# Optimization experiments

Measured on AMD Instinct MI355X. Metric: run time of the kernel, lower is better.

## Reference

```python
import jax, jax.numpy as jnp
import numpy as np

N_NODES = 100000
N_EDGES = 1200000
IN_DIM, HID, OUT = 128, 64, 64


def setup_inputs() -> dict:
    key = jax.random.key(0)
    ks = jax.random.split(key, 16)
    s = 0.05
    return {
        "x": jax.random.normal(ks[0], (N_NODES, IN_DIM), jnp.float32),
        "fc_w": jax.random.normal(ks[1], (IN_DIM, HID), jnp.float32) * s,
        "fc_b": jnp.zeros((HID,), jnp.float32),
        "conv1_w": jax.random.normal(ks[2], (IN_DIM, HID), jnp.float32) * s,
        "conv1_b": jnp.zeros((HID,), jnp.float32),
        "fc1_w": jax.random.normal(ks[3], (2 * HID, OUT), jnp.float32) * s,
        "fc1_b": jnp.zeros((OUT,), jnp.float32),
        "conv2_w": jax.random.normal(ks[4], (2 * HID, OUT), jnp.float32) * s,
        "conv2_b": jnp.zeros((OUT,), jnp.float32),
        "fc2_w": jax.random.normal(ks[5], (OUT, 1), jnp.float32) * s,
        "fc2_b": jnp.zeros((1,), jnp.float32),
        "conv3_w": jax.random.normal(ks[6], (OUT, 1), jnp.float32) * s,
        "conv3_b": jnp.zeros((1,), jnp.float32),
        "edge_index": jax.random.randint(ks[7], (2, N_EDGES), 0, N_NODES, jnp.int64 if jax.config.jax_enable_x64 else jnp.int32),
    }


def gcn_conv(h_in, w, b, row, col, norm, n_nodes):
    # PyG GCNConv (no self loops): scatter_add(norm * (XW)[row]) at col, + bias
    h = h_in @ w                                  # [N, F_out]
    msg = h[row] * norm[:, None]                  # [E, F_out]
    out = jax.ops.segment_sum(msg, col, num_segments=n_nodes)
    return out + b


def reference(x, fc_w, fc_b, conv1_w, conv1_b, fc1_w, fc1_b, conv2_w, conv2_b,
              fc2_w, fc2_b, conv3_w, conv3_b, edge_index):
    n = x.shape[0]
    row, col = edge_index[0], edge_index[1]
    # symmetric normalization: deg over destination nodes (unit edge weights)
    deg = jax.ops.segment_sum(jnp.ones(row.shape[0], x.dtype), col, num_segments=n)
    dinv = jnp.where(deg > 0, jax.lax.rsqrt(jnp.maximum(deg, 1.0)), 0.0)
    norm = dinv[row] * dinv[col]                  # [E]

    x1 = jax.nn.relu(x @ fc_w + fc_b)             # MLP branch [N, HID]
    x2 = jax.nn.relu(gcn_conv(x, conv1_w, conv1_b, row, col, norm, n))
    x3 = jnp.concatenate([x1, x2], axis=1)        # [N, 2*HID]
    x5 = jax.nn.relu(x3 @ fc1_w + fc1_b)
    x6 = jax.nn.relu(gcn_conv(x3, conv2_w, conv2_b, row, col, norm, n))
    x7 = x5 + x6                                  # residual combine [N, OUT]
    x9 = x7 @ fc2_w + fc2_b
    x10 = gcn_conv(x7, conv3_w, conv3_b, row, col, norm, n)
    return x9 + x10                               # [N, 1]
```

## Files before the change

### kernel.cpp

```cpp
#include <hip/hip_runtime.h>

#define IN_DIM 128
#define HID 64
#define RB_SHIFT 10
#define RB 1024
#define NBMAX 128
#define MAXBIN 16384
#define PCH 2048

typedef short bf16x8 __attribute__((ext_vector_type(8)));
typedef float f32x4  __attribute__((ext_vector_type(4)));

__device__ __forceinline__ float relu(float v) { return v > 0.f ? v : 0.f; }

__device__ __forceinline__ unsigned short f2bf(float f) {
    unsigned u = __float_as_uint(f);
    u += 0x7FFFu + ((u >> 16) & 1u);
    return (unsigned short)(u >> 16);
}

__device__ __forceinline__ float bflo(unsigned u) { return __uint_as_float(u << 16); }
__device__ __forceinline__ float bfhi(unsigned u) { return __uint_as_float(u & 0xFFFF0000u); }

__global__ void k_initbins(int* __restrict__ binCursor, int NR) {
    if (threadIdx.x < NR) binCursor[threadIdx.x] = threadIdx.x * MAXBIN;
}

__global__ __launch_bounds__(256) void k_wprep(const float* __restrict__ W1a,
                                               const float* __restrict__ W2a,
                                               const float* __restrict__ W1b,
                                               const float* __restrict__ W2b,
                                               unsigned short* __restrict__ Wt) {
    const int t = blockIdx.x * 256 + threadIdx.x;
    if (t >= 2 * 4 * 8 * 64) return;
    const int lane = t & 63;
    const int c = (t >> 6) & 7;
    const int kc = (t >> 9) & 3;
    const int layer = t >> 11;
    const int col = c * 16 + (lane & 15);
    const int k0 = kc * 32 + (lane >> 4) * 8;
    const float* W1 = layer ? W1b : W1a;
    const float* W2 = layer ? W2b : W2a;
    const float* src = (col < 64) ? (W1 + col) : (W2 + (col - 64));
    unsigned short v[8];
#pragma unroll
    for (int j = 0; j < 8; j++) v[j] = f2bf(src[(size_t)(k0 + j) * 64]);
    *(ushort4*)(Wt + (size_t)t * 8) = make_ushort4(v[0], v[1], v[2], v[3]);
    *(ushort4*)(Wt + (size_t)t * 8 + 4) = make_ushort4(v[4], v[5], v[6], v[7]);
}

__global__ __launch_bounds__(256) void k_part(const int* __restrict__ row,
                                              const int* __restrict__ col,
                                              int* __restrict__ binCursor,
                                              int2* __restrict__ part, int E) {
    __shared__ int lcur[NBMAX], gbase[NBMAX];
    const int tid = threadIdx.x;
    const int e0 = blockIdx.x * PCH;
    const int cnt = min(PCH, E - e0);
    if (tid < NBMAX) lcur[tid] = 0;
    __syncthreads();
    int rr[8], cc[8], pp[8];
    if (cnt == PCH) {
#pragma unroll
        for (int h = 0; h < 2; h++) {
            const int4 c4 = *(const int4*)(col + e0 + h * 1024 + tid * 4);
            const int4 r4 = *(const int4*)(row + e0 + h * 1024 + tid * 4);
            cc[h * 4 + 0] = c4.x; cc[h * 4 + 1] = c4.y;
            cc[h * 4 + 2] = c4.z; cc[h * 4 + 3] = c4.w;
            rr[h * 4 + 0] = r4.x; rr[h * 4 + 1] = r4.y;
            rr[h * 4 + 2] = r4.z; rr[h * 4 + 3] = r4.w;
        }
    } else {
#pragma unroll
        for (int j = 0; j < 8; j++) {
            const int e = e0 + j * 256 + tid;
            if (e < e0 + cnt) { rr[j] = row[e]; cc[j] = col[e]; }
            else cc[j] = -1;
        }
    }
#pragma unroll
    for (int j = 0; j < 8; j++)
        if (cc[j] >= 0) pp[j] = atomicAdd(&lcur[cc[j] >> RB_SHIFT], 1);
    __syncthreads();
    if (tid < NBMAX && lcur[tid] > 0)
        gbase[tid] = atomicAdd(&binCursor[tid], lcur[tid]);
    __syncthreads();
#pragma unroll
    for (int j = 0; j < 8; j++)
        if (cc[j] >= 0)
            part[gbase[cc[j] >> RB_SHIFT] + pp[j]] = make_int2(rr[j], cc[j]);
}

__global__ __launch_bounds__(256) void k_hist(const int* __restrict__ binCursor,
                                              const int2* __restrict__ part,
                                              int* __restrict__ degi,
                                              float* __restrict__ dinv, int N) {
    __shared__ int cnt[RB];
    const int b = blockIdx.x;
    const int lo = b << RB_SHIFT;
    const int tid = threadIdx.x;
    for (int i = tid; i < RB; i += 256) cnt[i] = 0;
    __syncthreads();
    const int base = b * MAXBIN;
    const int tot = binCursor[b] - base;
    for (int i = tid; i < tot; i += 256)
        atomicAdd(&cnt[part[base + i].y - lo], 1);
    __syncthreads();
    for (int i = tid; i < RB; i += 256) {
        const int n = lo + i;
        if (n < N) {
            const int d = cnt[i];
            degi[n] = d;
            dinv[n] = d > 0 ? rsqrtf((float)d) : 0.f;
        }
    }
}

__global__ __launch_bounds__(256) void k_scan1(const int* __restrict__ degi,
                                               int* __restrict__ start,
                                               int* __restrict__ bsum, int N) {
    __shared__ int s[256];
    const int tid = threadIdx.x;
    const int i = blockIdx.x * 256 + tid;
    const int v = (i < N) ? degi[i] : 0;
    s[tid] = v;
    __syncthreads();
    for (int off = 1; off < 256; off <<= 1) {
        int t = (tid >= off) ? s[tid - off] : 0;
        __syncthreads();
        s[tid] += t;
        __syncthreads();
    }
    if (i < N) start[i] = s[tid] - v;
    if (tid == 255) bsum[blockIdx.x] = s[255];
}

__global__ __launch_bounds__(512) void k_scan2(int* __restrict__ bsum, int NB) {
    __shared__ int s[512];
    const int tid = threadIdx.x;
    const int v = (tid < NB) ? bsum[tid] : 0;
    s[tid] = v;
    __syncthreads();
    for (int off = 1; off < 512; off <<= 1) {
        int t = (tid >= off) ? s[tid - off] : 0;
        __syncthreads();
        s[tid] += t;
        __syncthreads();
    }
    if (tid < NB) bsum[tid] = s[tid] - v;
}

__global__ __launch_bounds__(256) void k_scan3(int* __restrict__ start,
                                               const int* __restrict__ bsum, int N) {
    int i = blockIdx.x * 256 + threadIdx.x;
    if (i < N) start[i] += bsum[blockIdx.x];
}

__global__ __launch_bounds__(256) void k_bucket3(const int* __restrict__ binCursor,
                                                 const int2* __restrict__ part,
                                                 const int* __restrict__ start,
                                                 const float* __restrict__ dinv,
                                                 int2* __restrict__ rw, int N) {
    __shared__ int curs[RB];
    __shared__ float dv[RB];
    const int b = blockIdx.x;
    const int lo = b << RB_SHIFT;
    const int tid = threadIdx.x;
    for (int i = tid; i < RB; i += 256) {
        const int n = lo + i;
        curs[i] = (n < N) ? start[n] : 0;
        dv[i] = (n < N) ? dinv[n] : 0.f;
    }
    __syncthreads();
    const int base = b * MAXBIN;
    const int tot = binCursor[b] - base;
    for (int i = tid; i < tot; i += 256) {
        const int2 v = part[base + i];
        const int li = v.y - lo;
        const int pos = atomicAdd(&curs[li], 1);
        rw[pos] = make_int2(v.x, __float_as_int(dinv[v.x] * dv[li]));
    }
}

template <int LAYER>
__global__ __launch_bounds__(256) void k_gemm(const float* __restrict__ XA,
                                              const float* __restrict__ XB,
                                              const float* __restrict__ CB,
                                              const unsigned short* __restrict__ Wt,
                                              const float* __restrict__ B1,
                                              float* __restrict__ O1,
                                              unsigned short* __restrict__ O2,
                                              int N) {
    const int tid = threadIdx.x;
    const int wave = tid >> 6;
    const int lane = tid & 63;
    const int quad = lane >> 4;
    const int lm = lane & 15;
    const int n0 = blockIdx.x * 64 + wave * 16;
    if (n0 >= N) return;
    const int nrow = min(n0 + lm, N - 1);

    f32x4 acc[8];
#pragma unroll
    for (int c = 0; c < 8; c++) acc[c] = (f32x4){0.f, 0.f, 0.f, 0.f};

#pragma unroll
    for (int kc = 0; kc < 4; kc++) {
        const int k0 = kc * 32 + quad * 8;
        float4 q0, q1;
        if (LAYER == 1) {
            const float* s = XA + (size_t)nrow * IN_DIM + k0;
            q0 = *(const float4*)s;
            q1 = *(const float4*)(s + 4);
        } else {
            if (kc < 2) {
                const float* s = XA + (size_t)nrow * 64 + k0;
                q0 = *(const float4*)s;
                q1 = *(const float4*)(s + 4);
            } else {
                const int kb = k0 - 64;
                const float* s = XB + (size_t)nrow * 64 + kb;
                q0 = *(const float4*)s;
                q1 = *(const float4*)(s + 4);
                const float4 c0 = *(const float4*)(CB + kb);
                const float4 c1 = *(const float4*)(CB + kb + 4);
                q0.x = relu(q0.x + c0.x); q0.y = relu(q0.y + c0.y);
                q0.z = relu(q0.z + c0.z); q0.w = relu(q0.w + c0.w);
                q1.x = relu(q1.x + c1.x); q1.y = relu(q1.y + c1.y);
                q1.z = relu(q1.z + c1.z); q1.w = relu(q1.w + c1.w);
            }
        }
        bf16x8 a;
        a[0] = (short)f2bf(q0.x); a[1] = (short)f2bf(q0.y);
        a[2] = (short)f2bf(q0.z); a[3] = (short)f2bf(q0.w);
        a[4] = (short)f2bf(q1.x); a[5] = (short)f2bf(q1.y);
        a[6] = (short)f2bf(q1.z); a[7] = (short)f2bf(q1.w);
#pragma unroll
        for (int c = 0; c < 8; c++) {
            const bf16x8 b = *(const bf16x8*)(Wt + (size_t)((kc * 8 + c) * 64 + lane) * 8);
            acc[c] = __builtin_amdgcn_mfma_f32_16x16x32_bf16(a, b, acc[c], 0, 0, 0);
        }
    }

    const int nb = n0 + quad * 4;
#pragma unroll
    for (int c = 0; c < 4; c++) {
        const int col = c * 16 + lm;
        const float b = B1[col];
#pragma unroll
        for (int r = 0; r < 4; r++) {
            const int n = nb + r;
            if (n < N) O1[(size_t)n * 64 + col] = relu(acc[c][r] + b);
        }
    }
#pragma unroll
    for (int c = 4; c < 8; c++) {
        const int col = (c - 4) * 16 + lm;
#pragma unroll
        for (int r = 0; r < 4; r++) {
            const int n = nb + r;
            if (n < N) O2[(size_t)n * 64 + col] = f2bf(acc[c][r]);
        }
    }
}

__global__ __launch_bounds__(256) void k_gather64(const int* __restrict__ start,
                                                  const int* __restrict__ degi,
                                                  const int2* __restrict__ rw,
                                                  const unsigned short* __restrict__ H,
                                                  float* __restrict__ AGG, int N) {
    const int l = threadIdx.x & 15;
    const int d = blockIdx.x * 16 + (threadIdx.x >> 4);
    if (d >= N) return;
    int s = start[d];
    const int e2 = s + degi[d];
    float a0 = 0.f, a1 = 0.f, a2 = 0.f, a3 = 0.f;
    for (; s + 3 < e2; s += 4) {
        const int2 ea = rw[s], eb = rw[s + 1], ec = rw[s + 2], ed = rw[s + 3];
        const uint2 ua = *(const uint2*)(H + (size_t)ea.x * 64 + l * 4);
        const uint2 ub = *(const uint2*)(H + (size_t)eb.x * 64 + l * 4);
        const uint2 uc = *(const uint2*)(H + (size_t)ec.x * 64 + l * 4);
        const uint2 ud = *(const uint2*)(H + (size_t)ed.x * 64 + l * 4);
        const float wa = __int_as_float(ea.y), wb = __int_as_float(eb.y);
        const float wc = __int_as_float(ec.y), wd = __int_as_float(ed.y);
        a0 += wa * bflo(ua.x); a1 += wa * bfhi(ua.x);
        a2 += wa * bflo(ua.y); a3 += wa * bfhi(ua.y);
        a0 += wb * bflo(ub.x); a1 += wb * bfhi(ub.x);
        a2 += wb * bflo(ub.y); a3 += wb * bfhi(ub.y);
        a0 += wc * bflo(uc.x); a1 += wc * bfhi(uc.x);
        a2 += wc * bflo(uc.y); a3 += wc * bfhi(uc.y);
        a0 += wd * bflo(ud.x); a1 += wd * bfhi(ud.x);
        a2 += wd * bflo(ud.y); a3 += wd * bfhi(ud.y);
    }
    for (; s < e2; ++s) {
        const int2 ea = rw[s];
        const uint2 ua = *(const uint2*)(H + (size_t)ea.x * 64 + l * 4);
        const float wa = __int_as_float(ea.y);
        a0 += wa * bflo(ua.x); a1 += wa * bfhi(ua.x);
        a2 += wa * bflo(ua.y); a3 += wa * bfhi(ua.y);
    }
    *(float4*)(AGG + (size_t)d * 64 + l * 4) = make_float4(a0, a1, a2, a3);
}

__global__ __launch_bounds__(256) void k_combine(const float* __restrict__ X5,
                                                 const float* __restrict__ AGG2,
                                                 const float* __restrict__ CB2,
                                                 const float* __restrict__ FC2W,
                                                 const float* __restrict__ FC2B,
                                                 const float* __restrict__ C3W,
                                                 const float* __restrict__ C3B,
                                                 float* __restrict__ H3,
                                                 float* __restrict__ OUT, int N) {
    const int lane = threadIdx.x & 63;
    const int n = blockIdx.x * 4 + (threadIdx.x >> 6);
    if (n >= N) return;
    const size_t o = (size_t)n * 64 + lane;
    const float v = X5[o] + relu(AGG2[o] + CB2[lane]);
    float p9 = v * FC2W[lane];
    float p10 = v * C3W[lane];
#pragma unroll
    for (int s = 32; s >= 1; s >>= 1) {
        p9 += __shfl_xor(p9, s, 64);
        p10 += __shfl_xor(p10, s, 64);
    }
    if (lane == 0) {
        OUT[n] = p9 + FC2B[0] + C3B[0];
        H3[n] = p10;
    }
}

__global__ __launch_bounds__(256) void k_gather1f(const int* __restrict__ start,
                                                  const int* __restrict__ degi,
                                                  const int2* __restrict__ rw,
                                                  const float* __restrict__ H3,
                                                  float* __restrict__ OUT, int N) {
    const int d = blockIdx.x * 256 + threadIdx.x;
    if (d >= N) return;
    int s = start[d];
    const int e2 = s + degi[d];
    float acc = 0.f;
    for (; s + 1 < e2; s += 2) {
        const int2 a = rw[s], b = rw[s + 1];
        acc += H3[a.x] * __int_as_float(a.y);
        acc += H3[b.x] * __int_as_float(b.y);
    }
    if (s < e2) {
        const int2 a = rw[s];
        acc += H3[a.x] * __int_as_float(a.y);
    }
    OUT[d] += acc;
}

extern "C" void kernel_launch(void* const* d_in, const int* in_sizes, int n_in,
                              void* d_out, int out_size, void* d_ws, size_t ws_size,
                              hipStream_t stream) {
    const float* x    = (const float*)d_in[0];
    const float* fcw  = (const float*)d_in[1];
    const float* fcb  = (const float*)d_in[2];
    const float* c1w  = (const float*)d_in[3];
    const float* c1b  = (const float*)d_in[4];
    const float* f1w  = (const float*)d_in[5];
    const float* f1b  = (const float*)d_in[6];
    const float* c2w  = (const float*)d_in[7];
    const float* c2b  = (const float*)d_in[8];
    const float* f2w  = (const float*)d_in[9];
    const float* f2b  = (const float*)d_in[10];
    const float* c3w  = (const float*)d_in[11];
    const float* c3b  = (const float*)d_in[12];
    const int*   ei   = (const int*)d_in[13];

    const int N = in_sizes[0] / IN_DIM;
    const int E = in_sizes[13] / 2;
    const int* row = ei;
    const int* col = ei + E;
    float* out = (float*)d_out;

    const int NR = (N + RB - 1) >> RB_SHIFT;

    const size_t Npad = ((size_t)N + 127) & ~(size_t)127;
    const size_t Epad = ((size_t)E + 127) & ~(size_t)127;
    const size_t NF = (size_t)N * 64;
    int*   binCur = (int*)d_ws;
    int*   degi   = binCur + NBMAX;
    float* dinv   = (float*)(degi + Npad);
    int*   start  = (int*)(dinv + Npad);
    int*   bsum   = start + Npad;
    unsigned short* Wt = (unsigned short*)(bsum + 512);
    int2*  part   = (int2*)(Wt + 2 * 16384);
    int2*  rw     = part + (size_t)NR * MAXBIN;
    float* x1     = (float*)(rw + Epad);
    unsigned short* h1 = (unsigned short*)(x1 + NF);
    float* agg1   = (float*)(h1 + NF);
    float* x5     = agg1 + NF;
    unsigned short* h2 = h1;
    float* agg2   = x1;
    float* h3     = agg1;

    const int gN = (N + 255) / 256;
    const int NB = (N + 255) / 256;
    const int gG = (N + 63) / 64;
    const int gW = (N + 15) / 16;
    const int gC = (N + 3) / 4;
    const int gP = (E + PCH - 1) / PCH;

    k_initbins<<<1, NBMAX, 0, stream>>>(binCur, NR);
    k_wprep<<<16, 256, 0, stream>>>(fcw, c1w, f1w, c2w, Wt);
    k_part<<<gP, 256, 0, stream>>>(row, col, binCur, part, E);
    k_hist<<<NR, 256, 0, stream>>>(binCur, part, degi, dinv, N);
    k_scan1<<<NB, 256, 0, stream>>>(degi, start, bsum, N);
    k_scan2<<<1, 512, 0, stream>>>(bsum, NB);
    k_scan3<<<NB, 256, 0, stream>>>(start, bsum, N);
    k_bucket3<<<NR, 256, 0, stream>>>(binCur, part, start, dinv, rw, N);

    k_gemm<1><<<gG, 256, 0, stream>>>(x, nullptr, nullptr, Wt, fcb, x1, h1, N);
    k_gather64<<<gW, 256, 0, stream>>>(start, degi, rw, h1, agg1, N);

    k_gemm<2><<<gG, 256, 0, stream>>>(x1, agg1, c1b, Wt + 16384, f1b, x5, h2, N);
    k_gather64<<<gW, 256, 0, stream>>>(start, degi, rw, h2, agg2, N);

    k_combine<<<gC, 256, 0, stream>>>(x5, agg2, c2b, f2w, f2b, c3w, c3b, h3, out, N);
    k_gather1f<<<gN, 256, 0, stream>>>(start, degi, rw, h3, out, N);
}
```

Measured before the change: 310.6 us.

## Fuse CSR build scans, store bf16 intermediates, fuse combine into gather

Folds the bin-cursor init into the weight-prep kernel. Replaces the three-kernel global scan with a per-bin local scan, using the fixed MAXBIN region offsets for CSR start positions. Layer-1 and aggregation outputs are stored as bf16 with bias and ReLU applied in the gather, so the second GEMM reads bf16 directly. The combine kernel is merged into the second gather, and the final gather is unrolled by 4. Together these cut launch count and memory traffic, at the cost of extra bf16 rounding on x1 and x2 and an rw array sized by bin capacity.

```diff
diff --git a/kernel.cpp b/kernel.cpp
--- a/kernel.cpp
+++ b/kernel.cpp
@@ -18,19 +18,16 @@
     u += 0x7FFFu + ((u >> 16) & 1u);
     return (unsigned short)(u >> 16);
 }
-
 __device__ __forceinline__ float bflo(unsigned u) { return __uint_as_float(u << 16); }
 __device__ __forceinline__ float bfhi(unsigned u) { return __uint_as_float(u & 0xFFFF0000u); }
-
-__global__ void k_initbins(int* __restrict__ binCursor, int NR) {
-    if (threadIdx.x < NR) binCursor[threadIdx.x] = threadIdx.x * MAXBIN;
-}
 
 __global__ __launch_bounds__(256) void k_wprep(const float* __restrict__ W1a,
                                                const float* __restrict__ W2a,
                                                const float* __restrict__ W1b,
                                                const float* __restrict__ W2b,
-                                               unsigned short* __restrict__ Wt) {
+                                               unsigned short* __restrict__ Wt,
+                                               int* __restrict__ binCursor, int NR) {
+    if (blockIdx.x == 0 && threadIdx.x < NR) binCursor[threadIdx.x] = threadIdx.x * MAXBIN;
     const int t = blockIdx.x * 256 + threadIdx.x;
     if (t >= 2 * 4 * 8 * 64) return;
     const int lane = t & 63;
@@ -91,11 +88,13 @@
             part[gbase[cc[j] >> RB_SHIFT] + pp[j]] = make_int2(rr[j], cc[j]);
 }
 
-__global__ __launch_bounds__(256) void k_hist(const int* __restrict__ binCursor,
+__global__ __launch_bounds__(256) void k_csrA(const int* __restrict__ binCursor,
                                               const int2* __restrict__ part,
                                               int* __restrict__ degi,
-                                              float* __restrict__ dinv, int N) {
+                                              float* __restrict__ dinv,
+                                              int* __restrict__ start, int N) {
     __shared__ int cnt[RB];
+    __shared__ int psum[256];
     const int b = blockIdx.x;
     const int lo = b << RB_SHIFT;
     const int tid = threadIdx.x;
@@ -106,61 +105,36 @@
     for (int i = tid; i < tot; i += 256)
         atomicAdd(&cnt[part[base + i].y - lo], 1);
     __syncthreads();
-    for (int i = tid; i < RB; i += 256) {
-        const int n = lo + i;
+    const int i0 = tid * 4;
+    const int c0 = cnt[i0], c1 = cnt[i0 + 1], c2 = cnt[i0 + 2], c3 = cnt[i0 + 3];
+    const int s = c0 + c1 + c2 + c3;
+    psum[tid] = s;
+    __syncthreads();
+    for (int off = 1; off < 256; off <<= 1) {
+        int t = (tid >= off) ? psum[tid - off] : 0;
+        __syncthreads();
+        psum[tid] += t;
+        __syncthreads();
+    }
+    const int e = psum[tid] - s;
+    const int offs[4] = {e, e + c0, e + c0 + c1, e + c0 + c1 + c2};
+    const int cs[4] = {c0, c1, c2, c3};
+#pragma unroll
+    for (int j = 0; j < 4; j++) {
+        const int n = lo + i0 + j;
         if (n < N) {
-            const int d = cnt[i];
-            degi[n] = d;
-            dinv[n] = d > 0 ? rsqrtf((float)d) : 0.f;
-        }
-    }
-}
-
-__global__ __launch_bounds__(256) void k_scan1(const int* __restrict__ degi,
-                                               int* __restrict__ start,
-                                               int* __restrict__ bsum, int N) {
-    __shared__ int s[256];
-    const int tid = threadIdx.x;
-    const int i = blockIdx.x * 256 + tid;
-    const int v = (i < N) ? degi[i] : 0;
-    s[tid] = v;
-    __syncthreads();
-    for (int off = 1; off < 256; off <<= 1) {
-        int t = (tid >= off) ? s[tid - off] : 0;
-        __syncthreads();
-        s[tid] += t;
-        __syncthreads();
-    }
-    if (i < N) start[i] = s[tid] - v;
-    if (tid == 255) bsum[blockIdx.x] = s[255];
-}
-
-__global__ __launch_bounds__(512) void k_scan2(int* __restrict__ bsum, int NB) {
-    __shared__ int s[512];
-    const int tid = threadIdx.x;
-    const int v = (tid < NB) ? bsum[tid] : 0;
-    s[tid] = v;
-    __syncthreads();
-    for (int off = 1; off < 512; off <<= 1) {
-        int t = (tid >= off) ? s[tid - off] : 0;
-        __syncthreads();
-        s[tid] += t;
-        __syncthreads();
-    }
-    if (tid < NB) bsum[tid] = s[tid] - v;
-}
-
-__global__ __launch_bounds__(256) void k_scan3(int* __restrict__ start,
-                                               const int* __restrict__ bsum, int N) {
-    int i = blockIdx.x * 256 + threadIdx.x;
-    if (i < N) start[i] += bsum[blockIdx.x];
-}
-
-__global__ __launch_bounds__(256) void k_bucket3(const int* __restrict__ binCursor,
-                                                 const int2* __restrict__ part,
-                                                 const int* __restrict__ start,
-                                                 const float* __restrict__ dinv,
-                                                 int2* __restrict__ rw, int N) {
+            degi[n] = cs[j];
+            start[n] = base + offs[j];
+            dinv[n] = cs[j] > 0 ? rsqrtf((float)cs[j]) : 0.f;
+        }
+    }
+}
+
+__global__ __launch_bounds__(256) void k_csrB(const int* __restrict__ binCursor,
+                                              const int2* __restrict__ part,
+                                              const int* __restrict__ start,
+                                              const float* __restrict__ dinv,
+                                              int2* __restrict__ rw, int N) {
     __shared__ int curs[RB];
     __shared__ float dv[RB];
     const int b = blockIdx.x;
@@ -183,12 +157,13 @@
 }
 
 template <int LAYER>
-__global__ __launch_bounds__(256) void k_gemm(const float* __restrict__ XA,
-                                              const float* __restrict__ XB,
-                                              const float* __restrict__ CB,
+__global__ __launch_bounds__(256) void k_gemm(const float* __restrict__ XF,
+                                              const unsigned short* __restrict__ X1B,
+                                              const unsigned short* __restrict__ X2B,
                                               const unsigned short* __restrict__ Wt,
                                               const float* __restrict__ B1,
-                                              float* __restrict__ O1,
+                                              float* __restrict__ O1f,
+                                              unsigned short* __restrict__ O1b,
                                               unsigned short* __restrict__ O2,
                                               int N) {
     const int tid = threadIdx.x;
@@ -207,34 +182,20 @@
 #pragma unroll
     for (int kc = 0; kc < 4; kc++) {
         const int k0 = kc * 32 + quad * 8;
-        float4 q0, q1;
+        bf16x8 a;
         if (LAYER == 1) {
-            const float* s = XA + (size_t)nrow * IN_DIM + k0;
-            q0 = *(const float4*)s;
-            q1 = *(const float4*)(s + 4);
+            const float* s = XF + (size_t)nrow * IN_DIM + k0;
+            const float4 q0 = *(const float4*)s;
+            const float4 q1 = *(const float4*)(s + 4);
+            a[0] = (short)f2bf(q0.x); a[1] = (short)f2bf(q0.y);
+            a[2] = (short)f2bf(q0.z); a[3] = (short)f2bf(q0.w);
+            a[4] = (short)f2bf(q1.x); a[5] = (short)f2bf(q1.y);
+            a[6] = (short)f2bf(q1.z); a[7] = (short)f2bf(q1.w);
         } else {
-            if (kc < 2) {
-                const float* s = XA + (size_t)nrow * 64 + k0;
-                q0 = *(const float4*)s;
-                q1 = *(const float4*)(s + 4);
-            } else {
-                const int kb = k0 - 64;
-                const float* s = XB + (size_t)nrow * 64 + kb;
-                q0 = *(const float4*)s;
-                q1 = *(const float4*)(s + 4);
-                const float4 c0 = *(const float4*)(CB + kb);
-                const float4 c1 = *(const float4*)(CB + kb + 4);
-                q0.x = relu(q0.x + c0.x); q0.y = relu(q0.y + c0.y);
-                q0.z = relu(q0.z + c0.z); q0.w = relu(q0.w + c0.w);
-                q1.x = relu(q1.x + c1.x); q1.y = relu(q1.y + c1.y);
-                q1.z = relu(q1.z + c1.z); q1.w = relu(q1.w + c1.w);
-            }
-        }
-        bf16x8 a;
-        a[0] = (short)f2bf(q0.x); a[1] = (short)f2bf(q0.y);
-        a[2] = (short)f2bf(q0.z); a[3] = (short)f2bf(q0.w);
-        a[4] = (short)f2bf(q1.x); a[5] = (short)f2bf(q1.y);
-        a[6] = (short)f2bf(q1.z); a[7] = (short)f2bf(q1.w);
+            const unsigned short* s = (kc < 2) ? (X1B + (size_t)nrow * 64 + k0)
+                                               : (X2B + (size_t)nrow * 64 + (k0 - 64));
+            a = *(const bf16x8*)s;
+        }
 #pragma unroll
         for (int c = 0; c < 8; c++) {
             const bf16x8 b = *(const bf16x8*)(Wt + (size_t)((kc * 8 + c) * 64 + lane) * 8);
@@ -250,7 +211,11 @@
 #pragma unroll
         for (int r = 0; r < 4; r++) {
             const int n = nb + r;
-            if (n < N) O1[(size_t)n * 64 + col] = relu(acc[c][r] + b);
+            if (n < N) {
+                const float v = relu(acc[c][r] + b);
+                if (LAYER == 1) O1b[(size_t)n * 64 + col] = f2bf(v);
+                else            O1f[(size_t)n * 64 + col] = v;
+            }
         }
     }
 #pragma unroll
@@ -264,11 +229,20 @@
     }
 }
 
-__global__ __launch_bounds__(256) void k_gather64(const int* __restrict__ start,
-                                                  const int* __restrict__ degi,
-                                                  const int2* __restrict__ rw,
-                                                  const unsigned short* __restrict__ H,
-                                                  float* __restrict__ AGG, int N) {
+template <int MODE>
+__global__ __launch_bounds__(256) void k_gather(const int* __restrict__ start,
+                                                const int* __restrict__ degi,
+                                                const int2* __restrict__ rw,
+                                                const unsigned short* __restrict__ H,
+                                                const float* __restrict__ CB,
+                                                unsigned short* __restrict__ OXB,
+                                                const float* __restrict__ X5,
+                                                const float* __restrict__ FC2W,
+                                                const float* __restrict__ FC2B,
+                                                const float* __restrict__ C3W,
+                                                const float* __restrict__ C3B,
+                                                float* __restrict__ H3,
+                                                float* __restrict__ OUT, int N) {
     const int l = threadIdx.x & 15;
     const int d = blockIdx.x * 16 + (threadIdx.x >> 4);
     if (d >= N) return;
@@ -299,33 +273,31 @@
         a0 += wa * bflo(ua.x); a1 += wa * bfhi(ua.x);
         a2 += wa * bflo(ua.y); a3 += wa * bfhi(ua.y);
     }
-    *(float4*)(AGG + (size_t)d * 64 + l * 4) = make_float4(a0, a1, a2, a3);
-}
-
-__global__ __launch_bounds__(256) void k_combine(const float* __restrict__ X5,
-                                                 const float* __restrict__ AGG2,
-                                                 const float* __restrict__ CB2,
-                                                 const float* __restrict__ FC2W,
-                                                 const float* __restrict__ FC2B,
-                                                 const float* __restrict__ C3W,
-                                                 const float* __restrict__ C3B,
-                                                 float* __restrict__ H3,
-                                                 float* __restrict__ OUT, int N) {
-    const int lane = threadIdx.x & 63;
-    const int n = blockIdx.x * 4 + (threadIdx.x >> 6);
-    if (n >= N) return;
-    const size_t o = (size_t)n * 64 + lane;
-    const float v = X5[o] + relu(AGG2[o] + CB2[lane]);
-    float p9 = v * FC2W[lane];
-    float p10 = v * C3W[lane];
-#pragma unroll
-    for (int s = 32; s >= 1; s >>= 1) {
-        p9 += __shfl_xor(p9, s, 64);
-        p10 += __shfl_xor(p10, s, 64);
-    }
-    if (lane == 0) {
-        OUT[n] = p9 + FC2B[0] + C3B[0];
-        H3[n] = p10;
+    const float4 cb = *(const float4*)(CB + l * 4);
+    if (MODE == 1) {
+        ushort4 o;
+        o.x = f2bf(relu(a0 + cb.x)); o.y = f2bf(relu(a1 + cb.y));
+        o.z = f2bf(relu(a2 + cb.z)); o.w = f2bf(relu(a3 + cb.w));
+        *(ushort4*)(OXB + (size_t)d * 64 + l * 4) = o;
+    } else {
+        const float4 x5v = *(const float4*)(X5 + (size_t)d * 64 + l * 4);
+        const float v0 = x5v.x + relu(a0 + cb.x);
+        const float v1 = x5v.y + relu(a1 + cb.y);
+        const float v2 = x5v.z + relu(a2 + cb.z);
+        const float v3 = x5v.w + relu(a3 + cb.w);
+        const float4 w9 = *(const float4*)(FC2W + l * 4);
+        const float4 wX = *(const float4*)(C3W + l * 4);
+        float p9 = v0 * w9.x + v1 * w9.y + v2 * w9.z + v3 * w9.w;
+        float p10 = v0 * wX.x + v1 * wX.y + v2 * wX.z + v3 * wX.w;
+#pragma unroll
+        for (int m = 1; m < 16; m <<= 1) {
+            p9 += __shfl_xor(p9, m, 64);
+            p10 += __shfl_xor(p10, m, 64);
+        }
+        if (l == 0) {
+            OUT[d] = p9 + FC2B[0] + C3B[0];
+            H3[d] = p10;
+        }
     }
 }
 
@@ -339,12 +311,14 @@
     int s = start[d];
     const int e2 = s + degi[d];
     float acc = 0.f;
-    for (; s + 1 < e2; s += 2) {
-        const int2 a = rw[s], b = rw[s + 1];
+    for (; s + 3 < e2; s += 4) {
+        const int2 a = rw[s], b = rw[s + 1], c = rw[s + 2], e = rw[s + 3];
         acc += H3[a.x] * __int_as_float(a.y);
         acc += H3[b.x] * __int_as_float(b.y);
-    }
-    if (s < e2) {
+        acc += H3[c.x] * __int_as_float(c.y);
+        acc += H3[e.x] * __int_as_float(e.y);
+    }
+    for (; s < e2; ++s) {
         const int2 a = rw[s];
         acc += H3[a.x] * __int_as_float(a.y);
     }
@@ -378,46 +352,41 @@
     const int NR = (N + RB - 1) >> RB_SHIFT;
 
     const size_t Npad = ((size_t)N + 127) & ~(size_t)127;
-    const size_t Epad = ((size_t)E + 127) & ~(size_t)127;
     const size_t NF = (size_t)N * 64;
+    const size_t REG = (size_t)NR * MAXBIN;
     int*   binCur = (int*)d_ws;
     int*   degi   = binCur + NBMAX;
     float* dinv   = (float*)(degi + Npad);
     int*   start  = (int*)(dinv + Npad);
-    int*   bsum   = start + Npad;
-    unsigned short* Wt = (unsigned short*)(bsum + 512);
+    unsigned short* Wt = (unsigned short*)(start + Npad);
     int2*  part   = (int2*)(Wt + 2 * 16384);
-    int2*  rw     = part + (size_t)NR * MAXBIN;
-    float* x1     = (float*)(rw + Epad);
-    unsigned short* h1 = (unsigned short*)(x1 + NF);
-    float* agg1   = (float*)(h1 + NF);
-    float* x5     = agg1 + NF;
+    int2*  rw     = part + REG;
+    unsigned short* x1bf = (unsigned short*)(rw + REG);
+    unsigned short* h1   = x1bf + NF;
+    unsigned short* x2bf = h1 + NF;
+    float* x5     = (float*)(x2bf + NF);
+    float* h3     = x5 + NF;
     unsigned short* h2 = h1;
-    float* agg2   = x1;
-    float* h3     = agg1;
 
     const int gN = (N + 255) / 256;
-    const int NB = (N + 255) / 256;
     const int gG = (N + 63) / 64;
     const int gW = (N + 15) / 16;
-    const int gC = (N + 3) / 4;
     const int gP = (E + PCH - 1) / PCH;
 
-    k_initbins<<<1, NBMAX, 0, stream>>>(binCur, NR);
-    k_wprep<<<16, 256, 0, stream>>>(fcw, c1w, f1w, c2w, Wt);
+    k_wprep<<<16, 256, 0, stream>>>(fcw, c1w, f1w, c2w, Wt, binCur, NR);
     k_part<<<gP, 256, 0, stream>>>(row, col, binCur, part, E);
-    k_hist<<<NR, 256, 0, stream>>>(binCur, part, degi, dinv, N);
-    k_scan1<<<NB, 256, 0, stream>>>(degi, start, bsum, N);
-    k_scan2<<<1, 512, 0, stream>>>(bsum, NB);
-    k_scan3<<<NB, 256, 0, stream>>>(start, bsum, N);
-    k_bucket3<<<NR, 256, 0, stream>>>(binCur, part, start, dinv, rw, N);
-
-    k_gemm<1><<<gG, 256, 0, stream>>>(x, nullptr, nullptr, Wt, fcb, x1, h1, N);
-    k_gather64<<<gW, 256, 0, stream>>>(start, degi, rw, h1, agg1, N);
-
-    k_gemm<2><<<gG, 256, 0, stream>>>(x1, agg1, c1b, Wt + 16384, f1b, x5, h2, N);
-    k_gather64<<<gW, 256, 0, stream>>>(start, degi, rw, h2, agg2, N);
-
-    k_combine<<<gC, 256, 0, stream>>>(x5, agg2, c2b, f2w, f2b, c3w, c3b, h3, out, N);
+    k_csrA<<<NR, 256, 0, stream>>>(binCur, part, degi, dinv, start, N);
+    k_csrB<<<NR, 256, 0, stream>>>(binCur, part, start, dinv, rw, N);
+
+    k_gemm<1><<<gG, 256, 0, stream>>>(x, nullptr, nullptr, Wt, fcb,
+                                      nullptr, x1bf, h1, N);
+    k_gather<1><<<gW, 256, 0, stream>>>(start, degi, rw, h1, c1b, x2bf,
+                                        nullptr, nullptr, nullptr, nullptr,
+                                        nullptr, nullptr, nullptr, N);
+
+    k_gemm<2><<<gG, 256, 0, stream>>>(nullptr, x1bf, x2bf, Wt + 16384, f1b,
+                                      x5, nullptr, h2, N);
+    k_gather<2><<<gW, 256, 0, stream>>>(start, degi, rw, h2, c2b, nullptr,
+                                        x5, f2w, f2b, c3w, c3b, h3, out, N);
     k_gather1f<<<gN, 256, 0, stream>>>(start, degi, rw, h3, out, N);
 }
```

Result: faster. 285.5 us (-8.1%).
